# Optimization experiments

Measured on AMD Instinct MI355X. Metric: run time of the kernel, lower is better.

The kernel has to match this reference:

```python
import jax, jax.numpy as jnp
import numpy as np

TEMPERATURE_F = 0.5  # temperature_f from __init__


def setup_inputs() -> dict:
    key = jax.random.key(0)
    k1, k2 = jax.random.split(key)
    B, D = 4096, 512
    h_i = jax.random.normal(k1, (B, D), dtype=jnp.float32)
    h_j = jax.random.normal(k2, (B, D), dtype=jnp.float32)
    return {"h_i": h_i, "h_j": h_j}


def reference(h_i, h_j) -> jnp.ndarray:
    # NT-Xent loss (forward_private). N = 2*batch_size.
    B = h_i.shape[0]
    N = 2 * B
    h = jnp.concatenate([h_i, h_j], axis=0)          # [N, D]
    sim = (h @ h.T) / TEMPERATURE_F                   # [N, N]

    # Positive pairs: sim[i, i+B] and sim[i+B, i]
    sim_i_j = jnp.diagonal(sim, offset=B)             # [B]
    sim_j_i = jnp.diagonal(sim, offset=-B)            # [B]
    pos = jnp.concatenate([sim_i_j, sim_j_i], axis=0)  # [N]

    # Original builds logits = [pos | negatives] where negatives are the row of
    # sim with the diagonal and the positive entry removed, and labels are 0.
    # Cross-entropy per row = -pos_i + logsumexp(pos_i, negatives_i)
    #                       = -pos_i + logsumexp over row i of sim excluding the
    #                         diagonal (the positive entry equals pos_i, so the
    #                         set of logsumexp'd values is identical).
    neg_inf = jnp.finfo(sim.dtype).min
    diag = jnp.eye(N, dtype=bool)
    sim_masked = jnp.where(diag, neg_inf, sim)        # exclude self-similarity
    lse = jax.nn.logsumexp(sim_masked, axis=1)        # [N]

    loss = jnp.sum(lse - pos) / N                     # CE sum reduction, / N
    return loss
```

## Files before the change

### kernel.cpp

```cpp
#include <hip/hip_runtime.h>
#include <hip/hip_bf16.h>
#include <float.h>

#define BN_ 4096
#define DD  512
#define NN  8192
#define SCALE 2.0f
#define BUF 16384

typedef unsigned short u16;
typedef __attribute__((ext_vector_type(8))) short short8;
typedef __attribute__((ext_vector_type(4))) float floatx4;

struct alignas(8) U16x4 { u16 x, y, z, w; };

__device__ __forceinline__ u16 f2bf(float f) {
    union { float f; unsigned u; } c; c.f = f;
    unsigned u = c.u;
    unsigned r = (u + 0x7fffu + ((u >> 16) & 1u)) >> 16;
    return (u16)r;
}

__device__ __forceinline__ void async_copy16(const u16* g, u16* l) {
    __builtin_amdgcn_global_load_lds(
        (const __attribute__((address_space(1))) void*)g,
        (__attribute__((address_space(3))) void*)l, 16, 0, 0);
}

__global__ __launch_bounds__(256) void convert_pos_kernel(const float* __restrict__ hi,
                                                          const float* __restrict__ hj,
                                                          u16* __restrict__ H,
                                                          float* __restrict__ Pos,
                                                          float* __restrict__ out) {
    __shared__ float red[4];
    int t = blockIdx.x * 256 + threadIdx.x;
    int e = t * 4;
    const int BD = BN_ * DD;
    float4 a = *(const float4*)(hi + e);
    float4 b = *(const float4*)(hj + e);
    U16x4 oa, ob;
    oa.x = f2bf(a.x); oa.y = f2bf(a.y); oa.z = f2bf(a.z); oa.w = f2bf(a.w);
    ob.x = f2bf(b.x); ob.y = f2bf(b.y); ob.z = f2bf(b.z); ob.w = f2bf(b.w);
    *(U16x4*)(H + e) = oa;
    *(U16x4*)(H + BD + e) = ob;
    float dot = a.x * b.x + a.y * b.y + a.z * b.z + a.w * b.w;
#pragma unroll
    for (int msk = 1; msk < 64; msk <<= 1) dot += __shfl_xor(dot, msk);
    int lane = threadIdx.x & 63, wid = threadIdx.x >> 6;
    if (lane == 0) red[wid] = dot;
    __syncthreads();
    if (threadIdx.x == 0) {
        Pos[blockIdx.x] = red[0] + red[1] + red[2] + red[3];
        if (blockIdx.x == 0) *out = 0.0f;
    }
}

#define LD8(buf, kk, off) (*(const short8*)&(buf)[(kk) * 8192 + (off)])
#define MFMA_(va, vb, c) __builtin_amdgcn_mfma_f32_16x16x32_bf16(va, vb, c, 0, 0, 0)

#define MF_ROW(mi, areg)                       \
    acc[mi][0] = MFMA_(areg, b0, acc[mi][0]);  \
    acc[mi][1] = MFMA_(areg, b1, acc[mi][1]);  \
    acc[mi][2] = MFMA_(areg, b2, acc[mi][2]);  \
    acc[mi][3] = MFMA_(areg, b3, acc[mi][3]);

#define STAGE2(srcp, dstp) {                   \
    async_copy16((srcp) + s0, (dstp) + d0);    \
    async_copy16((srcp) + s1, (dstp) + d1); }

#define PHASE(kk, mh, RB, STG)                                   \
    {                                                            \
        short8 a0 = LD8(cA, kk, offA[(mh)*4 + 0]);               \
        short8 a1 = LD8(cA, kk, offA[(mh)*4 + 1]);               \
        short8 a2 = LD8(cA, kk, offA[(mh)*4 + 2]);               \
        short8 a3 = LD8(cA, kk, offA[(mh)*4 + 3]);               \
        if (RB) {                                                \
            b0 = LD8(cB, kk, offB[0]);                           \
            b1 = LD8(cB, kk, offB[1]);                           \
            b2 = LD8(cB, kk, offB[2]);                           \
            b3 = LD8(cB, kk, offB[3]);                           \
        }                                                        \
        STG;                                                     \
        asm volatile("s_waitcnt vmcnt(8)" ::: "memory");         \
        __builtin_amdgcn_s_barrier();                            \
        asm volatile("" ::: "memory");                           \
        __builtin_amdgcn_s_setprio(1);                           \
        MF_ROW((mh)*4 + 0, a0)                                   \
        MF_ROW((mh)*4 + 1, a1)                                   \
        MF_ROW((mh)*4 + 2, a2)                                   \
        MF_ROW((mh)*4 + 3, a3)                                   \
        __builtin_amdgcn_s_setprio(0);                           \
        __builtin_amdgcn_s_barrier();                            \
        asm volatile("" ::: "memory");                           \
    }

__global__ __launch_bounds__(512, 2) void gram_kernel(const u16* __restrict__ H,
                                                      float* __restrict__ Mpart,
                                                      float* __restrict__ Spart) {
    __shared__ u16 As[2 * BUF];
    __shared__ u16 Bs[2 * BUF];

    const int tid  = threadIdx.x;
    const int lane = tid & 63;
    const int wid  = tid >> 6;
    const int quad = lane >> 4;
    const int ln15 = lane & 15;
    const int wr = wid >> 2;
    const int wc = wid & 3;

    int t = blockIdx.x;
    int bi = (int)((sqrtf(8.0f * (float)t + 1.0f) - 1.0f) * 0.5f);
    while ((bi + 1) * (bi + 2) / 2 <= t) bi++;
    while (bi * (bi + 1) / 2 > t) bi--;
    const int bj = t - bi * (bi + 1) / 2;
    const bool diag = (bi == bj);
    const int biBase = bi * 256, bjBase = bj * 256;

    const u16* __restrict__ HA = H + (size_t)biBase * DD;
    const u16* __restrict__ HB = H + (size_t)bjBase * DD;

    const int c0 = tid,       r0 = c0 >> 2, p0 = c0 & 3;
    const int c1 = 512 + tid, r1 = c1 >> 2, p1 = c1 & 3;
    const int s0 = r0 * DD + ((p0 ^ (r0 & 3)) * 8), d0 = c0 * 8;
    const int s1 = r1 * DD + ((p1 ^ (r1 & 3)) * 8), d1 = c1 * 8;

    int offA[8], offB[4];
#pragma unroll
    for (int m = 0; m < 8; m++) {
        int r = wr * 128 + m * 16 + ln15;
        offA[m] = (r * 4 + (quad ^ (r & 3))) * 8;
    }
#pragma unroll
    for (int n = 0; n < 4; n++) {
        int r = wc * 64 + n * 16 + ln15;
        offB[n] = (r * 4 + (quad ^ (r & 3))) * 8;
    }

    floatx4 acc[8][4];
#pragma unroll
    for (int i = 0; i < 8; i++)
#pragma unroll
        for (int j = 0; j < 4; j++) acc[i][j] = (floatx4)0.0f;

    STAGE2(HA,      &As[0]);
    STAGE2(HA + 32, &As[8192]);
    STAGE2(HB,      &Bs[0]);
    STAGE2(HB + 32, &Bs[8192]);
    STAGE2(HA + 64, &As[BUF]);
    STAGE2(HB + 64, &Bs[BUF]);
    asm volatile("s_waitcnt vmcnt(4)" ::: "memory");
    __builtin_amdgcn_s_barrier();
    asm volatile("" ::: "memory");

#pragma unroll 2
    for (int kt = 0; kt < 8; ++kt) {
        u16* cA = &As[(kt & 1) * BUF];
        u16* cB = &Bs[(kt & 1) * BUF];
        u16* nA = &As[((kt + 1) & 1) * BUF];
        u16* nB = &Bs[((kt + 1) & 1) * BUF];
        const int kn1 = (kt + 1) * 64, kn2 = (kt + 2) * 64;
        short8 b0, b1, b2, b3;
        PHASE(0, 0, 1, if (kt < 7) STAGE2(HA + kn1 + 32, nA + 8192))
        PHASE(0, 1, 0, if (kt < 7) STAGE2(HB + kn1 + 32, nB + 8192))
        PHASE(1, 0, 1, if (kt < 6) STAGE2(HA + kn2,      cA))
        PHASE(1, 1, 0, if (kt < 6) STAGE2(HB + kn2,      cB))
    }

    asm volatile("s_waitcnt vmcnt(0)" ::: "memory");
    __syncthreads();

#pragma unroll
    for (int m = 0; m < 8; m++)
#pragma unroll
        for (int n = 0; n < 4; n++)
#pragma unroll
            for (int g = 0; g < 4; g++) {
                float v = SCALE * acc[m][n][g];
                if (diag) {
                    int lrow = wr * 128 + m * 16 + quad * 4 + g;
                    int lcol = wc * 64 + n * 16 + ln15;
                    if (lrow == lcol) v = -FLT_MAX;
                }
                acc[m][n][g] = v;
            }

    float* Rm = (float*)&As[0];
    float* Rs = Rm + 1024;
    float* Cm = Rs + 1024;
    float* Cs = Cm + 512;

#pragma unroll
    for (int m = 0; m < 8; m++) {
#pragma unroll
        for (int g = 0; g < 4; g++) {
            float vmax = fmaxf(fmaxf(acc[m][0][g], acc[m][1][g]),
                               fmaxf(acc[m][2][g], acc[m][3][g]));
#pragma unroll
            for (int msk = 1; msk < 16; msk <<= 1)
                vmax = fmaxf(vmax, __shfl_xor(vmax, msk));
            float s = __expf(acc[m][0][g] - vmax) + __expf(acc[m][1][g] - vmax)
                    + __expf(acc[m][2][g] - vmax) + __expf(acc[m][3][g] - vmax);
#pragma unroll
            for (int msk = 1; msk < 16; msk <<= 1) s += __shfl_xor(s, msk);
            if (ln15 == 0) {
                int x = wr * 128 + m * 16 + quad * 4 + g;
                Rm[wc * 256 + x] = vmax; Rs[wc * 256 + x] = s;
            }
        }
    }

    if (!diag) {
#pragma unroll
        for (int n = 0; n < 4; n++) {
            float cm = -FLT_MAX;
#pragma unroll
            for (int m = 0; m < 8; m++)
#pragma unroll
                for (int g = 0; g < 4; g++) cm = fmaxf(cm, acc[m][n][g]);
            cm = fmaxf(cm, __shfl_xor(cm, 16));
            cm = fmaxf(cm, __shfl_xor(cm, 32));
            float s = 0.0f;
#pragma unroll
            for (int m = 0; m < 8; m++)
#pragma unroll
                for (int g = 0; g < 4; g++) s += __expf(acc[m][n][g] - cm);
            s += __shfl_xor(s, 16);
            s += __shfl_xor(s, 32);
            if (quad == 0) {
                int y = wc * 64 + n * 16 + ln15;
                Cm[wr * 256 + y] = cm; Cs[wr * 256 + y] = s;
            }
        }
    }
    __syncthreads();

    if (tid < 256) {
        float m0 = Rm[tid], m1 = Rm[256 + tid], m2 = Rm[512 + tid], m3 = Rm[768 + tid];
        float mm = fmaxf(fmaxf(m0, m1), fmaxf(m2, m3));
        float s = Rs[tid] * __expf(m0 - mm) + Rs[256 + tid] * __expf(m1 - mm)
                + Rs[512 + tid] * __expf(m2 - mm) + Rs[768 + tid] * __expf(m3 - mm);
        Mpart[(size_t)bj * NN + biBase + tid] = mm;
        Spart[(size_t)bj * NN + biBase + tid] = s;
    } else if (!diag) {
        int y = tid - 256;
        float m0 = Cm[y], m1 = Cm[256 + y];
        float mm = fmaxf(m0, m1);
        float s = Cs[y] * __expf(m0 - mm) + Cs[256 + y] * __expf(m1 - mm);
        Mpart[(size_t)bi * NN + bjBase + y] = mm;
        Spart[(size_t)bi * NN + bjBase + y] = s;
    }
}

__global__ __launch_bounds__(256) void lse_kernel(const float* __restrict__ Mpart,
                                                  const float* __restrict__ Spart,
                                                  const float* __restrict__ Pos,
                                                  float* __restrict__ out) {
    __shared__ float sm[4][64], ss[4][64];
    __shared__ float red[256];
    int tid = threadIdx.x;
    int wid = tid >> 6, lane = tid & 63;
    int r = blockIdx.x * 64 + lane;
    float m = -FLT_MAX, s = 0.0f;
#pragma unroll
    for (int i = 0; i < 8; i++) {
        int c = wid * 8 + i;
        float mc = Mpart[(size_t)c * NN + r];
        float sc = Spart[(size_t)c * NN + r];
        float mn = fmaxf(m, mc);
        s = s * __expf(m - mn) + sc * __expf(mc - mn);
        m = mn;
    }
    sm[wid][lane] = m; ss[wid][lane] = s;
    __syncthreads();
    float v = 0.0f;
    if (tid < 64) {
        float m0 = sm[0][tid], m1 = sm[1][tid], m2 = sm[2][tid], m3 = sm[3][tid];
        float mm = fmaxf(fmaxf(m0, m1), fmaxf(m2, m3));
        float sa = ss[0][tid] * __expf(m0 - mm) + ss[1][tid] * __expf(m1 - mm)
                 + ss[2][tid] * __expf(m2 - mm) + ss[3][tid] * __expf(m3 - mm);
        v = mm + logf(sa);
        if (tid < 16) v += -4.0f * Pos[blockIdx.x * 16 + tid];
    }
    red[tid] = v;
    __syncthreads();
    for (int st = 128; st > 0; st >>= 1) {
        if (tid < st) red[tid] += red[tid + st];
        __syncthreads();
    }
    if (tid == 0) atomicAdd(out, red[0] * (1.0f / (float)NN));
}

extern "C" void kernel_launch(void* const* d_in, const int* in_sizes, int n_in,
                              void* d_out, int out_size, void* d_ws, size_t ws_size,
                              hipStream_t stream) {
    const float* hi = (const float*)d_in[0];
    const float* hj = (const float*)d_in[1];
    float* out = (float*)d_out;

    u16*   H     = (u16*)d_ws;
    float* Mpart = (float*)((char*)d_ws + (size_t)8 * 1024 * 1024);
    float* Spart = (float*)((char*)d_ws + (size_t)10 * 1024 * 1024);
    float* Pos   = (float*)((char*)d_ws + (size_t)12 * 1024 * 1024);

    convert_pos_kernel<<<2048, 256, 0, stream>>>(hi, hj, H, Pos, out);

    gram_kernel<<<528, 512, 0, stream>>>(H, Mpart, Spart);

    lse_kernel<<<128, 256, 0, stream>>>(Mpart, Spart, Pos, out);
}
```

Baseline: 158.6 us.

## Restructure LDS tile layout to 64-wide rows with 8-way XOR swizzle and reordered staging

Changes the shared-memory tile layout from two 32-column K halves to a single 64-column row-major tile with an 8-way XOR swizzle, so each global row chunk is staged contiguously. The prefetch schedule is rewritten to stage half-tiles by row blocks in a new order, with per-phase vmcnt waits. Clamped k offsets keep the loop branch-free, at the cost of redundant loads on the final iterations. The intent is fewer LDS bank conflicts and simpler, more regular async copies, but it risks subtle ordering hazards in the double buffer.

```diff
diff --git a/kernel.cpp b/kernel.cpp
--- a/kernel.cpp
+++ b/kernel.cpp
@@ -55,7 +55,6 @@
     }
 }
 
-#define LD8(buf, kk, off) (*(const short8*)&(buf)[(kk) * 8192 + (off)])
 #define MFMA_(va, vb, c) __builtin_amdgcn_mfma_f32_16x16x32_bf16(va, vb, c, 0, 0, 0)
 
 #define MF_ROW(mi, areg)                       \
@@ -64,24 +63,26 @@
     acc[mi][2] = MFMA_(areg, b2, acc[mi][2]);  \
     acc[mi][3] = MFMA_(areg, b3, acc[mi][3]);
 
-#define STAGE2(srcp, dstp) {                   \
-    async_copy16((srcp) + s0, (dstp) + d0);    \
-    async_copy16((srcp) + s1, (dstp) + d1); }
-
-#define PHASE(kk, mh, RB, STG)                                   \
+#define VMWAIT(n) asm volatile("s_waitcnt vmcnt(" #n ")" ::: "memory")
+
+#define STAGE(gb, k0, rbase, lb) {                                              \
+    async_copy16((gb) + (size_t)(rbase) * DD + (k0) + so0, (lb) + (rbase) * 64 + do0); \
+    async_copy16((gb) + (size_t)(rbase) * DD + (k0) + so1, (lb) + (rbase) * 64 + do1); }
+
+#define PHASE(cA, cB, kkq, mh, RB, STG, VMn)                     \
     {                                                            \
-        short8 a0 = LD8(cA, kk, offA[(mh)*4 + 0]);               \
-        short8 a1 = LD8(cA, kk, offA[(mh)*4 + 1]);               \
-        short8 a2 = LD8(cA, kk, offA[(mh)*4 + 2]);               \
-        short8 a3 = LD8(cA, kk, offA[(mh)*4 + 3]);               \
+        short8 a0 = *(const short8*)&cA[offA[kkq][(mh)*4 + 0]];  \
+        short8 a1 = *(const short8*)&cA[offA[kkq][(mh)*4 + 1]];  \
+        short8 a2 = *(const short8*)&cA[offA[kkq][(mh)*4 + 2]];  \
+        short8 a3 = *(const short8*)&cA[offA[kkq][(mh)*4 + 3]];  \
         if (RB) {                                                \
-            b0 = LD8(cB, kk, offB[0]);                           \
-            b1 = LD8(cB, kk, offB[1]);                           \
-            b2 = LD8(cB, kk, offB[2]);                           \
-            b3 = LD8(cB, kk, offB[3]);                           \
+            b0 = *(const short8*)&cB[offB[kkq][0]];              \
+            b1 = *(const short8*)&cB[offB[kkq][1]];              \
+            b2 = *(const short8*)&cB[offB[kkq][2]];              \
+            b3 = *(const short8*)&cB[offB[kkq][3]];              \
         }                                                        \
         STG;                                                     \
-        asm volatile("s_waitcnt vmcnt(8)" ::: "memory");         \
+        VMWAIT(VMn);                                             \
         __builtin_amdgcn_s_barrier();                            \
         asm volatile("" ::: "memory");                           \
         __builtin_amdgcn_s_setprio(1);                           \
@@ -119,21 +120,24 @@
     const u16* __restrict__ HA = H + (size_t)biBase * DD;
     const u16* __restrict__ HB = H + (size_t)bjBase * DD;
 
-    const int c0 = tid,       r0 = c0 >> 2, p0 = c0 & 3;
-    const int c1 = 512 + tid, r1 = c1 >> 2, p1 = c1 & 3;
-    const int s0 = r0 * DD + ((p0 ^ (r0 & 3)) * 8), d0 = c0 * 8;
-    const int s1 = r1 * DD + ((p1 ^ (r1 & 3)) * 8), d1 = c1 * 8;
-
-    int offA[8], offB[4];
-#pragma unroll
-    for (int m = 0; m < 8; m++) {
-        int r = wr * 128 + m * 16 + ln15;
-        offA[m] = (r * 4 + (quad ^ (r & 3))) * 8;
-    }
-#pragma unroll
-    for (int n = 0; n < 4; n++) {
-        int r = wc * 64 + n * 16 + ln15;
-        offB[n] = (r * 4 + (quad ^ (r & 3))) * 8;
+    const int c0 = tid, c1 = tid + 512;
+    const size_t so0 = (size_t)(c0 >> 3) * DD + ((c0 & 7) ^ ((c0 >> 3) & 7)) * 8;
+    const size_t so1 = (size_t)(c1 >> 3) * DD + ((c1 & 7) ^ ((c1 >> 3) & 7)) * 8;
+    const int do0 = c0 * 8, do1 = c1 * 8;
+
+    int offA[2][8], offB[2][4];
+#pragma unroll
+    for (int kk = 0; kk < 2; kk++) {
+#pragma unroll
+        for (int m = 0; m < 8; m++) {
+            int r = wr * 128 + m * 16 + ln15;
+            offA[kk][m] = (r * 8 + ((kk * 4 + quad) ^ (r & 7))) * 8;
+        }
+#pragma unroll
+        for (int n = 0; n < 4; n++) {
+            int r = wc * 64 + n * 16 + ln15;
+            offB[kk][n] = (r * 8 + ((kk * 4 + quad) ^ (r & 7))) * 8;
+        }
     }
 
     floatx4 acc[8][4];
@@ -142,13 +146,12 @@
 #pragma unroll
         for (int j = 0; j < 4; j++) acc[i][j] = (floatx4)0.0f;
 
-    STAGE2(HA,      &As[0]);
-    STAGE2(HA + 32, &As[8192]);
-    STAGE2(HB,      &Bs[0]);
-    STAGE2(HB + 32, &Bs[8192]);
-    STAGE2(HA + 64, &As[BUF]);
-    STAGE2(HB + 64, &Bs[BUF]);
-    asm volatile("s_waitcnt vmcnt(4)" ::: "memory");
+    STAGE(HB, 0,  0,   &Bs[0]);
+    STAGE(HB, 0,  128, &Bs[0]);
+    STAGE(HA, 0,  0,   &As[0]);
+    STAGE(HA, 0,  128, &As[0]);
+    STAGE(HB, 64, 0,   &Bs[BUF]);
+    VMWAIT(4);
     __builtin_amdgcn_s_barrier();
     asm volatile("" ::: "memory");
 
@@ -158,12 +161,13 @@
         u16* cB = &Bs[(kt & 1) * BUF];
         u16* nA = &As[((kt + 1) & 1) * BUF];
         u16* nB = &Bs[((kt + 1) & 1) * BUF];
-        const int kn1 = (kt + 1) * 64, kn2 = (kt + 2) * 64;
+        int k1 = (kt + 1) * 64; if (k1 > 448) k1 = 448;
+        int k2 = (kt + 2) * 64; if (k2 > 448) k2 = 448;
         short8 b0, b1, b2, b3;
-        PHASE(0, 0, 1, if (kt < 7) STAGE2(HA + kn1 + 32, nA + 8192))
-        PHASE(0, 1, 0, if (kt < 7) STAGE2(HB + kn1 + 32, nB + 8192))
-        PHASE(1, 0, 1, if (kt < 6) STAGE2(HA + kn2,      cA))
-        PHASE(1, 1, 0, if (kt < 6) STAGE2(HB + kn2,      cB))
+        PHASE(cA, cB, 0, 0, 1, STAGE(HB, k1, 128, nB), 4)
+        PHASE(cA, cB, 0, 1, 0, STAGE(HA, k1, 0,   nA), 8)
+        PHASE(cA, cB, 1, 0, 1, STAGE(HA, k1, 128, nA), 8)
+        PHASE(cA, cB, 1, 1, 0, STAGE(HB, k2, 0,   cB), 4)
     }
 
     asm volatile("s_waitcnt vmcnt(0)" ::: "memory");
```

Measured after the change: 156.9 us. About the same (-1.0%).
